# Optimization experiments

Measured on AMD Instinct MI355X. Metric: run time of the kernel, lower is better.

Reference implementation:

```python
import jax, jax.numpy as jnp
import numpy as np

SCALE = 1.0
DENSE = 4
ITERS = 5


def setup_inputs() -> dict:
    key = jax.random.key(0)
    k1, k2, k3 = jax.random.split(key, 3)
    data = jax.random.normal(k1, (8, 32, 512, 512), dtype=jnp.float32)
    # nonnegative marginal attention maps (strictly positive to keep sums safe)
    attx = jax.random.uniform(k2, (8, 512, 1), dtype=jnp.float32, minval=0.01, maxval=1.0)
    atty = jax.random.uniform(k3, (8, 512, 1), dtype=jnp.float32, minval=0.01, maxval=1.0)
    return {"data": data, "attx": attx, "atty": atty}


def _axis_coords(att, out_size):
    """Iterative clipped inverse-CDF sampling coords (AttSamplerGrid math).

    att: (N, S) nonnegative marginal attention. Returns coords in [-1, 1], (N, out_size).
    """
    N, S = att.shape
    att = att / jnp.sum(att, axis=1, keepdims=True) * out_size  # sum == out_size
    thr = DENSE * out_size / S  # each input cell maps to at most `dense` output pixels
    for _ in range(ITERS):
        att = jnp.minimum(att, thr)
        # redistribute clipped mass uniformly so the sum returns to out_size
        att = att + (out_size - jnp.sum(att, axis=1, keepdims=True)) / S
    csum = jnp.cumsum(att, axis=1)                      # (N, S) monotone CDF * out_size
    step = csum[:, -1:] / out_size                      # (N, 1), ~1.0
    tgt = step * jnp.arange(1, out_size + 1, dtype=att.dtype)[None, :]  # (N, out)
    # first index j with csum[j] >= target  (inverse CDF)
    j = jax.vmap(lambda c, t: jnp.searchsorted(c, t, side='left'))(csum, tgt)
    j = jnp.clip(j, 0, S - 1)
    right = jnp.take_along_axis(csum, j, axis=1)
    left = jnp.where(j > 0, jnp.take_along_axis(csum, jnp.maximum(j - 1, 0), axis=1), 0.0)
    frac = jnp.clip((tgt - left) / jnp.maximum(right - left, 1e-8), 0.0, 1.0)
    return (j.astype(att.dtype) + frac) / S * 2.0 - 1.0


def _lerp_axis(x, coord, axis):
    """1-D linear interpolation of x along `axis` at normalized coords in [-1,1].

    x: (N, C, H, W); coord: (N, L). align_corners=True mapping, coords stay in-range
    so zero-padding never triggers (bilinear grid_sample is separable for this grid).
    """
    size = x.shape[axis]
    p = (coord + 1.0) * 0.5 * (size - 1)
    p0f = jnp.floor(p)
    w = p - p0f                                         # (N, L)
    i0 = jnp.clip(p0f.astype(jnp.int32), 0, size - 1)
    i1 = jnp.clip(i0 + 1, 0, size - 1)
    shp = [coord.shape[0], 1, 1, 1]
    shp[axis] = coord.shape[1]
    i0 = i0.reshape(shp)
    i1 = i1.reshape(shp)
    w = w.reshape(shp)
    x0 = jnp.take_along_axis(x, i0, axis=axis)
    x1 = jnp.take_along_axis(x, i1, axis=axis)
    return x0 * (1.0 - w) + x1 * w


def reference(data, attx, atty):
    N, C, H, W = data.shape
    out_h = int(round(H * SCALE))
    out_w = int(round(W * SCALE))
    gx = _axis_coords(attx[..., 0], out_w)   # (N, out_w) x-coords (width)
    gy = _axis_coords(atty[..., 0], out_h)   # (N, out_h) y-coords (height)
    cols = _lerp_axis(data, gx, axis=3)      # (N, C, H, out_w)
    out = _lerp_axis(cols, gy, axis=2)       # (N, C, out_h, out_w)
    return out
```

## Files before the change

### kernel.cpp

```cpp
#include <hip/hip_runtime.h>

#define S    512
#define OUT  512
#define NB   8
#define CB   32
#define TRW  8
#define WPB  2
#define NBLK (NB * CB * 32)

__global__ __launch_bounds__(64) void coords_kernel(
    const float* __restrict__ attx, const float* __restrict__ atty,
    int2* __restrict__ coords)
{
  __shared__ double sc[S];
  const int lane = threadIdx.x;
  const int n    = blockIdx.x & 7;
  const int axis = blockIdx.x >> 3;
  const float* att = (axis == 0 ? attx : atty) + n * S;

  double a[8];
#pragma unroll
  for (int k = 0; k < 8; ++k) a[k] = (double)att[lane * 8 + k];

  double tot = 0.0;
#pragma unroll
  for (int k = 0; k < 8; ++k) tot += a[k];
#pragma unroll
  for (int off = 32; off > 0; off >>= 1) tot += __shfl_xor(tot, off);

#pragma unroll
  for (int k = 0; k < 8; ++k) a[k] = a[k] / tot * (double)OUT;
  const double thr = (double)(4 * OUT) / (double)S;

  for (int it = 0; it < 5; ++it) {
    double s = 0.0;
#pragma unroll
    for (int k = 0; k < 8; ++k) { a[k] = a[k] < thr ? a[k] : thr; s += a[k]; }
#pragma unroll
    for (int off = 32; off > 0; off >>= 1) s += __shfl_xor(s, off);
    const double corr = ((double)OUT - s) / (double)S;
#pragma unroll
    for (int k = 0; k < 8; ++k) a[k] += corr;
  }

  double p[8]; double run = 0.0;
#pragma unroll
  for (int k = 0; k < 8; ++k) { run += a[k]; p[k] = run; }
  double v = run;
#pragma unroll
  for (int off = 1; off < 64; off <<= 1) {
    double t = __shfl_up(v, off);
    if (lane >= off) v += t;
  }
  const double excl = v - run;
#pragma unroll
  for (int k = 0; k < 8; ++k) sc[lane * 8 + k] = excl + p[k];
  __syncthreads();

  const double step = sc[S - 1] / (double)OUT;

#pragma unroll
  for (int k = 0; k < 8; ++k) {
    const int ox = lane * 8 + k;
    const double tgt = step * (double)(ox + 1);

    int lo = 0, hi = S;
    while (lo < hi) {
      int mid = (lo + hi) >> 1;
      if (sc[mid] < tgt) lo = mid + 1; else hi = mid;
    }
    int j = lo < S - 1 ? lo : S - 1;

    double right = sc[j];
    double left  = (j > 0) ? sc[j - 1] : 0.0;
    double denom = right - left;
    if (denom < 1e-8) denom = 1e-8;
    double frac = (tgt - left) / denom;
    frac = frac < 0.0 ? 0.0 : (frac > 1.0 ? 1.0 : frac);

    double pp  = ((double)j + frac) / (double)S * (double)(S - 1);
    double p0f = floor(pp);
    double w   = pp - p0f;
    int i0 = (int)p0f;
    i0 = i0 < 0 ? 0 : (i0 > S - 1 ? S - 1 : i0);

    coords[(axis * NB + n) * S + ox] = make_int2(i0, __float_as_int((float)w));
  }
}

__global__ __launch_bounds__(128) void sample_kernel(
    const float* __restrict__ data, const int2* __restrict__ coords,
    float* __restrict__ out)
{
  __shared__ float bufA_[WPB][S + 1];
  __shared__ float bufB_[WPB][S + 1];

  int b = (int)blockIdx.x;
  b = (b & 7) * (NBLK / 8) + (b >> 3);
  const int plane = b >> 5;
  const int bip   = b & 31;
  const int n     = plane >> 5;

  const int tid  = threadIdx.x;
  const int wv   = tid >> 6;
  const int lane = tid & 63;
  const int oy0  = (bip * WPB + wv) * TRW;

  const float* __restrict__ pl = data + (size_t)plane * (S * S);
  float* __restrict__       po = out  + (size_t)plane * (S * S);

  int   ix[8];
  float wx[8];
#pragma unroll
  for (int k = 0; k < 8; ++k) {
    const int2 cx = coords[n * S + lane + 64 * k];
    ix[k] = cx.x;
    wx[k] = __int_as_float(cx.y);
  }

  float* bufA = bufA_[wv];
  float* bufB = bufB_[wv];
  const int2* __restrict__ cyp = coords + (NB + n) * S + oy0;

  float CxA[8], CxB[8];
  int curA = -1000;

  for (int r = 0; r < TRW; ++r) {
    const int2 cy = cyp[r];
    const int   a  = cy.x;
    const float wy = __int_as_float(cy.y);

    if (a != curA) {
      const int rowB = (a + 1 < S) ? a + 1 : S - 1;
      if (a == curA + 1) {
#pragma unroll
        for (int k = 0; k < 8; ++k) CxA[k] = CxB[k];
        const float4* RB = (const float4*)(pl + (size_t)rowB * S);
        const float4 p0 = RB[lane];
        const float4 p1 = RB[lane + 64];
        ((float4*)bufB)[lane]      = p0;
        ((float4*)bufB)[lane + 64] = p1;
        if (lane == 63) bufB[S] = p1.w;
#pragma unroll
        for (int k = 0; k < 8; ++k) {
          const float x0 = bufB[ix[k]];
          const float x1 = bufB[ix[k] + 1];
          CxB[k] = x0 + wx[k] * (x1 - x0);
        }
      } else {
        const float4* RA = (const float4*)(pl + (size_t)a    * S);
        const float4* RB = (const float4*)(pl + (size_t)rowB * S);
        const float4 q0 = RA[lane];
        const float4 q1 = RA[lane + 64];
        const float4 p0 = RB[lane];
        const float4 p1 = RB[lane + 64];
        ((float4*)bufA)[lane]      = q0;
        ((float4*)bufA)[lane + 64] = q1;
        ((float4*)bufB)[lane]      = p0;
        ((float4*)bufB)[lane + 64] = p1;
        if (lane == 63) { bufA[S] = q1.w; bufB[S] = p1.w; }
#pragma unroll
        for (int k = 0; k < 8; ++k) {
          const float x0 = bufA[ix[k]];
          const float x1 = bufA[ix[k] + 1];
          CxA[k] = x0 + wx[k] * (x1 - x0);
        }
#pragma unroll
        for (int k = 0; k < 8; ++k) {
          const float x0 = bufB[ix[k]];
          const float x1 = bufB[ix[k] + 1];
          CxB[k] = x0 + wx[k] * (x1 - x0);
        }
      }
      curA = a;
    }

    float* orow = po + (size_t)(oy0 + r) * OUT;
#pragma unroll
    for (int k = 0; k < 8; ++k)
      __builtin_nontemporal_store(CxA[k] + wy * (CxB[k] - CxA[k]),
                                  orow + lane + 64 * k);
  }
}

extern "C" void kernel_launch(void* const* d_in, const int* in_sizes, int n_in,
                              void* d_out, int out_size, void* d_ws, size_t ws_size,
                              hipStream_t stream) {
  const float* data = (const float*)d_in[0];
  const float* attx = (const float*)d_in[1];
  const float* atty = (const float*)d_in[2];
  float* out = (float*)d_out;

  int2* coords = (int2*)d_ws;

  coords_kernel<<<16, 64, 0, stream>>>(attx, atty, coords);

  sample_kernel<<<NBLK, 128, 0, stream>>>(data, coords, out);
}
```

Measured before the change: 99.04 us.

## Balance output-row segments across waves by estimated row-load cost

```diff
diff --git a/kernel.cpp b/kernel.cpp
--- a/kernel.cpp
+++ b/kernel.cpp
@@ -4,15 +4,17 @@
 #define OUT  512
 #define NB   8
 #define CB   32
-#define TRW  8
 #define WPB  2
-#define NBLK (NB * CB * 32)
+#define NSPP 64
+#define NBLK (NB * CB * (NSPP / WPB))
 
 __global__ __launch_bounds__(64) void coords_kernel(
     const float* __restrict__ attx, const float* __restrict__ atty,
-    int2* __restrict__ coords)
+    int2* __restrict__ coords,
+    int* __restrict__ bnd)
 {
   __shared__ double sc[S];
+  __shared__ int pr[S];
   const int lane = threadIdx.x;
   const int n    = blockIdx.x & 7;
   const int axis = blockIdx.x >> 3;
@@ -59,6 +61,7 @@
 
   const double step = sc[S - 1] / (double)OUT;
 
+  int i0s[8];
 #pragma unroll
   for (int k = 0; k < 8; ++k) {
     const int ox = lane * 8 + k;
@@ -83,14 +86,47 @@
     double w   = pp - p0f;
     int i0 = (int)p0f;
     i0 = i0 < 0 ? 0 : (i0 > S - 1 ? S - 1 : i0);
+    i0s[k] = i0;
 
     coords[(axis * NB + n) * S + ox] = make_int2(i0, __float_as_int((float)w));
+  }
+
+  if (axis == 1) {
+    const int fromPrev = __shfl_up(i0s[7], 1);
+    int prevv = (lane == 0) ? (i0s[0] - 2) : fromPrev;
+    int cinc[8]; int runc = 0;
+#pragma unroll
+    for (int k = 0; k < 8; ++k) {
+      const int d = i0s[k] - prevv;
+      const int c = 1 + (d <= 0 ? 0 : (d == 1 ? 1 : 2));
+      runc += c; cinc[k] = runc; prevv = i0s[k];
+    }
+    int vv = runc;
+#pragma unroll
+    for (int off = 1; off < 64; off <<= 1) {
+      const int t = __shfl_up(vv, off);
+      if (lane >= off) vv += t;
+    }
+    const int exclc = vv - runc;
+#pragma unroll
+    for (int k = 0; k < 8; ++k) pr[lane * 8 + k] = exclc + cinc[k];
+    __syncthreads();
+
+    const int Ctot = pr[S - 1];
+    const int tgt = (int)(((long long)lane * Ctot) / NSPP);
+    int lo = 0, hi = S;
+    while (lo < hi) {
+      const int mid = (lo + hi) >> 1;
+      if (pr[mid] <= tgt) lo = mid + 1; else hi = mid;
+    }
+    bnd[n * (NSPP + 1) + lane] = lo;
+    if (lane == 63) bnd[n * (NSPP + 1) + NSPP] = S;
   }
 }
 
 __global__ __launch_bounds__(128) void sample_kernel(
     const float* __restrict__ data, const int2* __restrict__ coords,
-    float* __restrict__ out)
+    const int* __restrict__ bnd, float* __restrict__ out)
 {
   __shared__ float bufA_[WPB][S + 1];
   __shared__ float bufB_[WPB][S + 1];
@@ -104,7 +140,9 @@
   const int tid  = threadIdx.x;
   const int wv   = tid >> 6;
   const int lane = tid & 63;
-  const int oy0  = (bip * WPB + wv) * TRW;
+  const int s    = bip * WPB + wv;
+  const int oy0   = bnd[n * (NSPP + 1) + s];
+  const int oyend = bnd[n * (NSPP + 1) + s + 1];
 
   const float* __restrict__ pl = data + (size_t)plane * (S * S);
   float* __restrict__       po = out  + (size_t)plane * (S * S);
@@ -120,13 +158,13 @@
 
   float* bufA = bufA_[wv];
   float* bufB = bufB_[wv];
-  const int2* __restrict__ cyp = coords + (NB + n) * S + oy0;
+  const int2* __restrict__ cyp = coords + (NB + n) * S;
 
   float CxA[8], CxB[8];
   int curA = -1000;
 
-  for (int r = 0; r < TRW; ++r) {
-    const int2 cy = cyp[r];
+  for (int oy = oy0; oy < oyend; ++oy) {
+    const int2 cy = cyp[oy];
     const int   a  = cy.x;
     const float wy = __int_as_float(cy.y);
 
@@ -175,7 +213,7 @@
       curA = a;
     }
 
-    float* orow = po + (size_t)(oy0 + r) * OUT;
+    float* orow = po + (size_t)oy * OUT;
 #pragma unroll
     for (int k = 0; k < 8; ++k)
       __builtin_nontemporal_store(CxA[k] + wy * (CxB[k] - CxA[k]),
@@ -192,8 +230,9 @@
   float* out = (float*)d_out;
 
   int2* coords = (int2*)d_ws;
-
-  coords_kernel<<<16, 64, 0, stream>>>(attx, atty, coords);
-
-  sample_kernel<<<NBLK, 128, 0, stream>>>(data, coords, out);
+  int*  bnd    = (int*)((char*)d_ws + 2 * NB * S * sizeof(int2));
+
+  coords_kernel<<<16, 64, 0, stream>>>(attx, atty, coords, bnd);
+
+  sample_kernel<<<NBLK, 128, 0, stream>>>(data, coords, bnd, out);
 }
```

After: 99.40 us. About the same (+0.4%).
